# Kernel tuning notes

Hardware: AMD Instinct MI355X
Metric: run time of the kernel (lower is better)

The kernel has to match this reference:

```python
import jax, jax.numpy as jnp
import numpy as np

H = 1024          # hidden_size
NH = 16           # num_attention_heads
HD = H // NH      # head_size
EPS = 1e-5


def setup_inputs() -> dict:
    key = jax.random.key(0)
    ks = jax.random.split(key, 5)
    # xavier_uniform bound for Linear(in, out): sqrt(6/(in+out))
    b_qkv = float(np.sqrt(6.0 / (H + 3 * H)))
    b_out = float(np.sqrt(6.0 / (H + H)))
    return {
        "hidden_states": jax.random.normal(ks[0], (2, 2048, H), dtype=jnp.float32),
        "ln_gamma": jnp.ones((H,), jnp.float32),
        "ln_beta": jnp.zeros((H,), jnp.float32),
        "W_qkv": jax.random.uniform(ks[1], (3 * H, H), jnp.float32, -b_qkv, b_qkv),
        "b_qkv": jnp.zeros((3 * H,), jnp.float32),
        "W_out": jax.random.uniform(ks[2], (H, H), jnp.float32, -b_out, b_out),
        "b_out": jnp.zeros((H,), jnp.float32),
    }


def _attn_block(x, ln_gamma, ln_beta, W_qkv, b_qkv, W_out, b_out):
    B, S, _ = x.shape
    # Pre-LN
    mu = jnp.mean(x, axis=-1, keepdims=True)
    var = jnp.mean(jnp.square(x - mu), axis=-1, keepdims=True)
    xn = (x - mu) / jnp.sqrt(var + EPS) * ln_gamma + ln_beta
    # fused QKV projection: [B,S,3H]
    qkv = jnp.einsum("bsh,oh->bso", xn, W_qkv) + b_qkv
    qkv = qkv.reshape(B, S, 3, NH, HD).transpose(2, 0, 3, 1, 4)  # [3,B,NH,S,HD]
    q, k, v = qkv[0], qkv[1], qkv[2]
    scores = jnp.einsum("bhqd,bhkd->bhqk", q, k) / jnp.sqrt(jnp.asarray(HD, x.dtype))
    probs = jax.nn.softmax(scores, axis=-1)
    ctx = jnp.einsum("bhqk,bhkd->bhqd", probs, v)
    ctx = ctx.transpose(0, 2, 1, 3).reshape(B, S, H)
    out = jnp.einsum("bsh,oh->bso", ctx, W_out) + b_out  # dropout: eval mode = identity
    return x + out


def reference(hidden_states, ln_gamma, ln_beta, W_qkv, b_qkv, W_out, b_out):
    return _attn_block(hidden_states, ln_gamma, ln_beta, W_qkv, b_qkv, W_out, b_out)
```

## Files before the change

kernel.cpp:

```cpp
#include <hip/hip_runtime.h>
#include <stdint.h>

typedef unsigned short u16;
typedef __attribute__((ext_vector_type(8))) short bf16x8;
typedef __attribute__((ext_vector_type(4))) float f32x4;
typedef __attribute__((ext_vector_type(4))) unsigned int u32x4;
typedef __attribute__((ext_vector_type(2))) unsigned int u32x2;
typedef __attribute__((ext_vector_type(4))) unsigned short u16x4;

#define QSCALE 0.18033688011112042f

typedef __attribute__((address_space(1))) const void gvoid;
typedef __attribute__((address_space(3))) void svoid;

__device__ __forceinline__ void cp16(const u16* g, u16* l) {
    __builtin_amdgcn_global_load_lds((gvoid*)g, (svoid*)l, 16, 0, 0);
}

__device__ __forceinline__ u16 f2bf(float f) {
    uint32_t u = __float_as_uint(f);
    u += 0x7fff + ((u >> 16) & 1);
    return (u16)(u >> 16);
}

__device__ __forceinline__ uint32_t pack_bf2(float lo, float hi) {
    uint32_t a = __float_as_uint(lo) + 0x8000u;
    uint32_t b = __float_as_uint(hi) + 0x8000u;
    return __builtin_amdgcn_perm(b, a, 0x07060302);
}

__global__ __launch_bounds__(256) void k_pre(const float* __restrict__ X,
                                             const float* __restrict__ gam,
                                             const float* __restrict__ bet,
                                             u16* __restrict__ XN,
                                             const float* __restrict__ Wqkv, u16* __restrict__ Wq,
                                             const float* __restrict__ Wout, u16* __restrict__ Wo) {
    __shared__ float red[8];
    const int bid = blockIdx.x;
    if (bid < 4096) {
        int t = bid;
        const float4* xp = (const float4*)(X + (size_t)t * 1024);
        float4 x = xp[threadIdx.x];
        float s  = x.x + x.y + x.z + x.w;
        float s2 = x.x*x.x + x.y*x.y + x.z*x.z + x.w*x.w;
        #pragma unroll
        for (int off = 1; off < 64; off <<= 1) {
            s  += __shfl_xor(s,  off, 64);
            s2 += __shfl_xor(s2, off, 64);
        }
        int lane = threadIdx.x & 63, w = threadIdx.x >> 6;
        if (lane == 0) { red[w] = s; red[w + 4] = s2; }
        __syncthreads();
        s  = red[0] + red[1] + red[2] + red[3];
        s2 = red[4] + red[5] + red[6] + red[7];
        float mu  = s * (1.0f / 1024.0f);
        float var = s2 * (1.0f / 1024.0f) - mu * mu;
        float rin = rsqrtf(var + 1e-5f);
        float4 g = ((const float4*)gam)[threadIdx.x];
        float4 b = ((const float4*)bet)[threadIdx.x];
        u16x4 o;
        o.x = f2bf((x.x - mu) * rin * g.x + b.x);
        o.y = f2bf((x.y - mu) * rin * g.y + b.y);
        o.z = f2bf((x.z - mu) * rin * g.z + b.z);
        o.w = f2bf((x.w - mu) * rin * g.w + b.w);
        *(u16x4*)(XN + (size_t)t * 1024 + threadIdx.x * 4) = o;
    } else {
        int i = (bid - 4096) * 256 + threadIdx.x;
        const float* src; u16* dst;
        if (i < 786432) { src = Wqkv; dst = Wq; }
        else            { i -= 786432; src = Wout; dst = Wo; }
        float4 v = ((const float4*)src)[i];
        u16x4 o;
        o.x = f2bf(v.x); o.y = f2bf(v.y); o.z = f2bf(v.z); o.w = f2bf(v.w);
        ((u16x4*)dst)[i] = o;
    }
}

__device__ __forceinline__ void gemm_bt_tile(const u16* __restrict__ A, const u16* __restrict__ Bm,
                                             int m0, int n0, u16* As, u16* Bs, f32x4 acc[4][4]) {
    const int tid = threadIdx.x;
    const int lane = tid & 63;
    const int wv = tid >> 6;
    const int qi = lane & 15, g = lane >> 4, swz = qi & 7;
    const int wr = (wv >> 1) * 64, wc = (wv & 1) * 64;
    #pragma unroll
    for (int mi = 0; mi < 4; mi++)
        #pragma unroll
        for (int ni = 0; ni < 4; ni++) acc[mi][ni] = (f32x4){0.f, 0.f, 0.f, 0.f};

    const int row_in = tid >> 3;
    const int cs = (tid & 7) ^ (row_in & 7);
    for (int k0 = 0; k0 < 1024; k0 += 64) {
        __syncthreads();
        #pragma unroll
        for (int i = 0; i < 4; i++) {
            int row = i * 32 + row_in;
            cp16(A  + (size_t)(m0 + row) * 1024 + k0 + cs * 8, As + (i * 256 + wv * 64) * 8);
            cp16(Bm + (size_t)(n0 + row) * 1024 + k0 + cs * 8, Bs + (i * 256 + wv * 64) * 8);
        }
        __syncthreads();
        #pragma unroll
        for (int ks = 0; ks < 2; ks++) {
            bf16x8 af[4], bf[4];
            #pragma unroll
            for (int mi = 0; mi < 4; mi++)
                af[mi] = *(const bf16x8*)(As + (wr + mi * 16 + qi) * 64 + ((ks * 4 + g) ^ swz) * 8);
            #pragma unroll
            for (int ni = 0; ni < 4; ni++)
                bf[ni] = *(const bf16x8*)(Bs + (wc + ni * 16 + qi) * 64 + ((ks * 4 + g) ^ swz) * 8);
            #pragma unroll
            for (int mi = 0; mi < 4; mi++)
                #pragma unroll
                for (int ni = 0; ni < 4; ni++)
                    acc[mi][ni] = __builtin_amdgcn_mfma_f32_16x16x32_bf16(af[mi], bf[ni], acc[mi][ni], 0, 0, 0);
        }
    }
}

__global__ __launch_bounds__(256) void k_qkv(const u16* __restrict__ XN, const u16* __restrict__ Wq,
                                             const float* __restrict__ bqkv,
                                             u16* __restrict__ Q, u16* __restrict__ K,
                                             u16* __restrict__ Vt) {
    __shared__ __align__(16) u16 SMEM[17408];
    u16* As = SMEM;
    u16* Bs = SMEM + 8192;
    f32x4 acc[4][4];
    const int m0 = blockIdx.y * 128, n0 = blockIdx.x * 128;
    gemm_bt_tile(XN, Wq, m0, n0, As, Bs, acc);
    const int lane = threadIdx.x & 63, wid = threadIdx.x >> 6;
    const int g = lane >> 4, qi = lane & 15;
    const int wr = (wid >> 1) * 64, wc = (wid & 1) * 64;
    if (n0 < 2048) {
        const int which = n0 >> 10;
        u16* base = which ? K : Q;
        const float scale = which ? 1.0f : QSCALE;
        #pragma unroll
        for (int mi = 0; mi < 4; mi++)
            #pragma unroll
            for (int ni = 0; ni < 4; ni++)
                #pragma unroll
                for (int i = 0; i < 4; i++) {
                    int m = m0 + wr + mi * 16 + (g * 4 + i);
                    int n = n0 + wc + ni * 16 + qi;
                    float v = (acc[mi][ni][i] + bqkv[n]) * scale;
                    int b = m >> 11, s = m & 2047;
                    int hh = (n >> 6) & 15, d = n & 63;
                    base[((size_t)(b * 16 + hh) * 2048 + s) * 64 + d] = f2bf(v);
                }
    } else {
        __syncthreads();
        u16* Tw = SMEM + wid * 4352;
        #pragma unroll
        for (int mi = 0; mi < 4; mi++)
            #pragma unroll
            for (int ni = 0; ni < 4; ni++) {
                int n = n0 + wc + ni * 16 + qi;
                float bq = bqkv[n];
                u16x4 pk;
                pk.x = f2bf(acc[mi][ni][0] + bq);
                pk.y = f2bf(acc[mi][ni][1] + bq);
                pk.z = f2bf(acc[mi][ni][2] + bq);
                pk.w = f2bf(acc[mi][ni][3] + bq);
                *(u16x4*)(Tw + (ni * 16 + qi) * 68 + mi * 16 + g * 4) = pk;
            }
        const int head = (n0 + wc - 2048) >> 6;
        const int b = m0 >> 11;
        const int s0 = (m0 + wr) & 2047;
        u16* vrow = Vt + (size_t)(b * 16 + head) * 64 * 2048 + s0 + qi * 4;
        #pragma unroll
        for (int dd = 0; dd < 16; dd++) {
            int d = dd * 4 + g;
            u16x4 val = *(const u16x4*)(Tw + d * 68 + qi * 4);
            *(u16x4*)(vrow + (size_t)d * 2048) = val;
        }
    }
}

__global__ __launch_bounds__(512) void k_attn(const u16* __restrict__ Q, const u16* __restrict__ K,
                                              const u16* __restrict__ Vt, u16* __restrict__ CTX) {
    __shared__ __align__(16) u16 Ks[2][64 * 64];
    __shared__ __align__(16) u16 Vs[2][64 * 64];
    __shared__ __align__(16) u16 Ps[8][16 * 64];
    const int id = blockIdx.x;
    const int bh = (id & 7) * 4 + ((id >> 3) & 3);
    const int q0 = (id >> 5) * 128;
    const int lane = threadIdx.x & 63, w = threadIdx.x >> 6;
    const int g = lane >> 4, qi = lane & 15, swz = qi & 7;
    const u16* Qp = Q  + (size_t)bh * (2048 * 64);
    const u16* Kp = K  + (size_t)bh * (2048 * 64);
    const u16* Vp = Vt + (size_t)bh * (64 * 2048);
    u16* Pw = Ps[w];

    const int r0 = w * 8 + (lane >> 3);
    const int cs = (lane & 7) ^ (r0 & 7);
    const u16* kg0 = Kp + (size_t)r0 * 64 + cs * 8;
    const u16* vg0 = Vp + (size_t)r0 * 2048 + cs * 8;

    bf16x8 bq[2];
    {
        const u16* qb = Qp + (size_t)(q0 + w * 16 + qi) * 64 + g * 8;
        bq[0] = *(const bf16x8*)(qb);
        bq[1] = *(const bf16x8*)(qb + 32);
    }
    float lsumA = 0.f, lsumB = 0.f;
    f32x4 od[4];
    #pragma unroll
    for (int nt = 0; nt < 4; nt++) od[nt] = (f32x4){0.f, 0.f, 0.f, 0.f};

    cp16(kg0, Ks[0] + w * 512);
    cp16(vg0, Vs[0] + w * 512);

    #define ATTN_STEP(KT, CKS, CVS, PKS, PVS)                                                    \
    {                                                                                            \
        const int kt_ = (KT);                                                                    \
        __syncthreads();                                                                         \
        if (kt_ < 31) {                                                                          \
            cp16(kg0 + 4096, (PKS) + w * 512);                 \
            cp16(vg0 + 64,   (PVS) + w * 512);            \
        }                                                                                        \
        const u16* ksp = (CKS);                                                                  \
        const u16* vsp = (CVS);                                                                  \
        f32x4 sv[4];                                                                             \
        _Pragma("unroll")                                                                        \
        for (int nt = 0; nt < 4; nt++) sv[nt] = (f32x4){0.f, 0.f, 0.f, 0.f};                     \
        _Pragma("unroll")                                                                        \
        for (int ks = 0; ks < 2; ks++)                                                           \
            _Pragma("unroll")                                                                    \
            for (int nt = 0; nt < 4; nt++) {                                                     \
                bf16x8 ak = *(const bf16x8*)(ksp + (nt * 16 + qi) * 64 + ((ks * 4 + g) ^ swz) * 8); \
                sv[nt] = __builtin_amdgcn_mfma_f32_16x16x32_bf16(ak, bq[ks], sv[nt], 0, 0, 0);   \
            }                                                                                    \
        _Pragma("unroll")                                                                        \
        for (int nt = 0; nt < 2; nt++) {                                                         \
            float e0 = __builtin_amdgcn_exp2f(sv[nt][0]);                                        \
            float e1 = __builtin_amdgcn_exp2f(sv[nt][1]);                                        \
            float e2 = __builtin_amdgcn_exp2f(sv[nt][2]);                                        \
            float e3 = __builtin_amdgcn_exp2f(sv[nt][3]);                                        \
            lsumA += e0 + e1; lsumB += e2 + e3;                                                  \
            u32x2 pk = {pack_bf2(e0, e1), pack_bf2(e2, e3)};                                     \
            *(u32x2*)(Pw + qi * 64 + ((2 * nt + (g >> 1)) ^ swz) * 8 + (g & 1) * 4) = pk;        \
        }                                                                                        \
        {                                                                                        \
            bf16x8 bp = *(const bf16x8*)(Pw + qi * 64 + ((0 * 4 + g) ^ swz) * 8);                \
            _Pragma("unroll")                                                                    \
            for (int nt = 0; nt < 4; nt++) {                                                     \
                bf16x8 av = *(const bf16x8*)(vsp + (nt * 16 + qi) * 64 + ((0 * 4 + g) ^ swz) * 8); \
                od[nt] = __builtin_amdgcn_mfma_f32_16x16x32_bf16(av, bp, od[nt], 0, 0, 0);       \
            }                                                                                    \
        }                                                                                        \
        _Pragma("unroll")                                                                        \
        for (int nt = 2; nt < 4; nt++) {                                                         \
            float e0 = __builtin_amdgcn_exp2f(sv[nt][0]);                                        \
            float e1 = __builtin_amdgcn_exp2f(sv[nt][1]);                                        \
            float e2 = __builtin_amdgcn_exp2f(sv[nt][2]);                                        \
            float e3 = __builtin_amdgcn_exp2f(sv[nt][3]);                                        \
            lsumA += e0 + e1; lsumB += e2 + e3;                                                  \
            u32x2 pk = {pack_bf2(e0, e1), pack_bf2(e2, e3)};                                     \
            *(u32x2*)(Pw + qi * 64 + ((2 * nt + (g >> 1)) ^ swz) * 8 + (g & 1) * 4) = pk;        \
        }                                                                                        \
        {                                                                                        \
            bf16x8 bp = *(const bf16x8*)(Pw + qi * 64 + ((1 * 4 + g) ^ swz) * 8);                \
            _Pragma("unroll")                                                                    \
            for (int nt = 0; nt < 4; nt++) {                                                     \
                bf16x8 av = *(const bf16x8*)(vsp + (nt * 16 + qi) * 64 + ((1 * 4 + g) ^ swz) * 8); \
                od[nt] = __builtin_amdgcn_mfma_f32_16x16x32_bf16(av, bp, od[nt], 0, 0, 0);       \
            }                                                                                    \
        }                                                                                        \
        kg0 += 64 * 64; vg0 += 64;                                                               \
    }

    for (int kt = 0; kt < 32; kt += 2) {
        ATTN_STEP(kt,     Ks[0], Vs[0], Ks[1], Vs[1]);
        ATTN_STEP(kt + 1, Ks[1], Vs[1], Ks[0], Vs[0]);
    }
    #undef ATTN_STEP

    float lsum = lsumA + lsumB;
    lsum += __shfl_xor(lsum, 16, 64);
    lsum += __shfl_xor(lsum, 32, 64);
    float inv = 1.0f / lsum;
    const int b = bh >> 4, hh = bh & 15;
    size_t m = (size_t)b * 2048 + q0 + w * 16 + qi;
    u16* cp = CTX + m * 1024 + hh * 64 + g * 4;
    #pragma unroll
    for (int nt = 0; nt < 4; nt++) {
        u16x4 o;
        o.x = f2bf(od[nt][0] * inv); o.y = f2bf(od[nt][1] * inv);
        o.z = f2bf(od[nt][2] * inv); o.w = f2bf(od[nt][3] * inv);
        *(u16x4*)(cp + nt * 16) = o;
    }
}

__global__ __launch_bounds__(256) void k_out(const u16* __restrict__ CTX, const u16* __restrict__ Wo,
                                             const float* __restrict__ bout, const float* __restrict__ X,
                                             float* __restrict__ OUT) {
    __shared__ __align__(16) u16 As[128 * 64], Bs[128 * 64];
    f32x4 acc[4][4];
    const int m0 = blockIdx.y * 128, n0 = blockIdx.x * 128;
    gemm_bt_tile(CTX, Wo, m0, n0, As, Bs, acc);
    const int lane = threadIdx.x & 63, wid = threadIdx.x >> 6;
    const int wr = (wid >> 1) * 64, wc = (wid & 1) * 64;
    #pragma unroll
    for (int mi = 0; mi < 4; mi++)
        #pragma unroll
        for (int ni = 0; ni < 4; ni++)
            #pragma unroll
            for (int i = 0; i < 4; i++) {
                size_t m = m0 + wr + mi * 16 + ((lane >> 4) * 4 + i);
                int n = n0 + wc + ni * 16 + (lane & 15);
                OUT[m * 1024 + n] = acc[mi][ni][i] + bout[n] + X[m * 1024 + n];
            }
}

extern "C" void kernel_launch(void* const* d_in, const int* in_sizes, int n_in,
                              void* d_out, int out_size, void* d_ws, size_t ws_size,
                              hipStream_t stream) {
    const float* X    = (const float*)d_in[0];
    const float* gam  = (const float*)d_in[1];
    const float* bet  = (const float*)d_in[2];
    const float* Wqkv = (const float*)d_in[3];
    const float* bqkv = (const float*)d_in[4];
    const float* Wout = (const float*)d_in[5];
    const float* bout = (const float*)d_in[6];
    float* OUT = (float*)d_out;

    u16* XN  = (u16*)d_ws;
    u16* Q   = XN  + (size_t)4 * 1024 * 1024;
    u16* K   = Q   + (size_t)4 * 1024 * 1024;
    u16* Vt  = K   + (size_t)4 * 1024 * 1024;
    u16* CTX = Vt  + (size_t)4 * 1024 * 1024;
    u16* Wq  = CTX + (size_t)4 * 1024 * 1024;
    u16* Wo  = Wq  + (size_t)3 * 1024 * 1024;

    k_pre<<<8192, 256, 0, stream>>>(X, gam, bet, XN, Wqkv, Wq, Wout, Wo);
    k_qkv<<<dim3(24, 32), 256, 0, stream>>>(XN, Wq, bqkv, Q, K, Vt);
    k_attn<<<512, 512, 0, stream>>>(Q, K, Vt, CTX);
    k_out<<<dim3(8, 32), 256, 0, stream>>>(CTX, Wo, bout, X, OUT);
}
```

Baseline: 200.6 us.

## Rewrite QKV GEMM as 256x256 tile with double-buffered phased pipeline

The QKV projection kernel moves from 128x128 tiles with 256 threads to 256x256 tiles with 512 threads and a swizzled 1D grid of 192 blocks. Its main loop becomes a hand-scheduled double-buffered pipeline: async global-to-LDS copies for the next k-steps are issued between MFMA phases, with explicit vmcnt/lgkmcnt waits, barriers and setprio around the MFMA bursts. The goal is more data reuse per tile and hiding load latency behind matrix math. In exchange it uses 128KB of LDS and 32 accumulators per thread, which raises register pressure and may limit occupancy. The V-transpose epilogue is split into two halves to fit the larger tile.

```diff
diff --git a/kernel.cpp b/kernel.cpp
--- a/kernel.cpp
+++ b/kernel.cpp
@@ -117,25 +117,116 @@
     }
 }
 
-__global__ __launch_bounds__(256) void k_qkv(const u16* __restrict__ XN, const u16* __restrict__ Wq,
-                                             const float* __restrict__ bqkv,
-                                             u16* __restrict__ Q, u16* __restrict__ K,
-                                             u16* __restrict__ Vt) {
-    __shared__ __align__(16) u16 SMEM[17408];
-    u16* As = SMEM;
-    u16* Bs = SMEM + 8192;
-    f32x4 acc[4][4];
-    const int m0 = blockIdx.y * 128, n0 = blockIdx.x * 128;
-    gemm_bt_tile(XN, Wq, m0, n0, As, Bs, acc);
-    const int lane = threadIdx.x & 63, wid = threadIdx.x >> 6;
-    const int g = lane >> 4, qi = lane & 15;
-    const int wr = (wid >> 1) * 64, wc = (wid & 1) * 64;
+
+#define CFENCE asm volatile("" ::: "memory")
+#define BARX() do { CFENCE; __builtin_amdgcn_s_barrier(); CFENCE; } while (0)
+#define LGKM0() asm volatile("s_waitcnt lgkmcnt(0)" ::: "memory")
+
+__global__ __launch_bounds__(512, 2) void k_qkv(const u16* __restrict__ XN, const u16* __restrict__ Wq,
+                                                const float* __restrict__ bqkv,
+                                                u16* __restrict__ Q, u16* __restrict__ K,
+                                                u16* __restrict__ Vt) {
+    __shared__ __align__(16) u16 SMEM[65536];
+    const int tid = threadIdx.x;
+    const int lane = tid & 63, w = tid >> 6;
+    const int qi = lane & 15, g = lane >> 4, swz = qi & 7;
+    const int wr = (w >> 2) * 128, wc = (w & 3) * 64;
+
+    const int id = blockIdx.x;
+    const int sw = (id & 7) * 24 + (id >> 3);
+    const int n0 = (sw % 12) * 256;
+    const int m0 = (sw / 12) * 256;
+
+    const int laneRow = lane >> 3, laneCg = lane & 7;
+    const int cs = laneCg ^ laneRow;
+    const int aw = (w & 3) * 8 + (w >> 2) * 128;
+    const u16* gA = XN + (size_t)(m0 + aw + laneRow) * 1024 + cs * 8;
+    const u16* gB = Wq + (size_t)(n0 + w * 8 + laneRow) * 1024 + cs * 8;
+
+#define SM_A(s) (SMEM + (s) * 32768)
+#define SM_B(s) (SMEM + (s) * 32768 + 16384)
+#define STAGE_A(tau, q, s) cp16(gA + (size_t)(q) * 32 * 1024 + (tau) * 64, SM_A(s) + ((q) * 32 + aw) * 64)
+#define STAGE_B(tau, part, s)                                                                       \
+    do { cp16(gB + (size_t)(part) * 128 * 1024 + (tau) * 64, SM_B(s) + ((part) * 128 + w * 8) * 64); \
+         cp16(gB + (size_t)((part) * 128 + 64) * 1024 + (tau) * 64,                                  \
+              SM_B(s) + ((part) * 128 + 64 + w * 8) * 64); } while (0)
+
+    f32x4 acc[8][4];
+    #pragma unroll
+    for (int mi = 0; mi < 8; mi++)
+        #pragma unroll
+        for (int ni = 0; ni < 4; ni++) acc[mi][ni] = (f32x4){0.f, 0.f, 0.f, 0.f};
+    bf16x8 bf[4][2];
+
+    STAGE_B(0, 0, 0); STAGE_B(0, 1, 0);
+    STAGE_A(0, 0, 0); STAGE_A(0, 1, 0); STAGE_A(0, 2, 0); STAGE_A(0, 3, 0);
+    STAGE_B(1, 0, 1); STAGE_B(1, 1, 1);
+    STAGE_A(1, 0, 1); STAGE_A(1, 1, 1);
+    asm volatile("s_waitcnt vmcnt(6)" ::: "memory");
+    BARX();
+
+#define PHASE_A(q)                                                                                   \
+    bf16x8 af[2][2];                                                                                 \
+    _Pragma("unroll") for (int m2 = 0; m2 < 2; m2++)                                                 \
+    _Pragma("unroll") for (int ks = 0; ks < 2; ks++)                                                 \
+        af[m2][ks] = *(const bf16x8*)(as_ + (wr + ((q) * 2 + m2) * 16 + qi) * 64 + (((ks * 4 + g) ^ swz)) * 8);
+
+#define DO_MFMA(q)                                                                                   \
+    __builtin_amdgcn_s_setprio(1);                                                                   \
+    _Pragma("unroll") for (int m2 = 0; m2 < 2; m2++)                                                 \
+    _Pragma("unroll") for (int ni = 0; ni < 4; ni++) {                                               \
+        acc[(q) * 2 + m2][ni] = __builtin_amdgcn_mfma_f32_16x16x32_bf16(af[m2][0], bf[ni][0], acc[(q) * 2 + m2][ni], 0, 0, 0); \
+        acc[(q) * 2 + m2][ni] = __builtin_amdgcn_mfma_f32_16x16x32_bf16(af[m2][1], bf[ni][1], acc[(q) * 2 + m2][ni], 0, 0, 0); \
+    }                                                                                                \
+    __builtin_amdgcn_s_setprio(0);
+
+    for (int t = 0; t < 16; t++) {
+        const int s = t & 1;
+        const u16* as_ = SM_A(s);
+        const u16* bs_ = SM_B(s);
+        {
+            PHASE_A(0)
+            #pragma unroll
+            for (int ni = 0; ni < 4; ni++)
+                #pragma unroll
+                for (int ks = 0; ks < 2; ks++)
+                    bf[ni][ks] = *(const bf16x8*)(bs_ + (wc + ni * 16 + qi) * 64 + ((ks * 4 + g) ^ swz) * 8);
+            if (t < 15) { STAGE_A(t + 1, 2, s ^ 1); STAGE_A(t + 1, 3, s ^ 1); }
+            BARX(); LGKM0();
+            DO_MFMA(0)
+            BARX();
+        }
+        {
+            PHASE_A(1)
+            if (t < 14) STAGE_B(t + 2, 0, s);
+            BARX(); LGKM0();
+            DO_MFMA(1)
+            BARX();
+        }
+        {
+            PHASE_A(2)
+            if (t < 14) STAGE_B(t + 2, 1, s);
+            BARX(); LGKM0();
+            DO_MFMA(2)
+            BARX();
+        }
+        {
+            PHASE_A(3)
+            if (t < 14) { STAGE_A(t + 2, 0, s); STAGE_A(t + 2, 1, s); }
+            BARX(); LGKM0();
+            DO_MFMA(3)
+            if (t < 14) { asm volatile("s_waitcnt vmcnt(6)" ::: "memory"); }
+            else        { asm volatile("s_waitcnt vmcnt(0)" ::: "memory"); }
+            BARX();
+        }
+    }
+
     if (n0 < 2048) {
         const int which = n0 >> 10;
         u16* base = which ? K : Q;
         const float scale = which ? 1.0f : QSCALE;
         #pragma unroll
-        for (int mi = 0; mi < 4; mi++)
+        for (int mi = 0; mi < 8; mi++)
             #pragma unroll
             for (int ni = 0; ni < 4; ni++)
                 #pragma unroll
@@ -143,37 +234,46 @@
                     int m = m0 + wr + mi * 16 + (g * 4 + i);
                     int n = n0 + wc + ni * 16 + qi;
                     float v = (acc[mi][ni][i] + bqkv[n]) * scale;
-                    int b = m >> 11, s = m & 2047;
+                    int b = m >> 11, ss = m & 2047;
                     int hh = (n >> 6) & 15, d = n & 63;
-                    base[((size_t)(b * 16 + hh) * 2048 + s) * 64 + d] = f2bf(v);
+                    base[((size_t)(b * 16 + hh) * 2048 + ss) * 64 + d] = f2bf(v);
                 }
     } else {
-        __syncthreads();
-        u16* Tw = SMEM + wid * 4352;
-        #pragma unroll
-        for (int mi = 0; mi < 4; mi++)
-            #pragma unroll
-            for (int ni = 0; ni < 4; ni++) {
-                int n = n0 + wc + ni * 16 + qi;
-                float bq = bqkv[n];
-                u16x4 pk;
-                pk.x = f2bf(acc[mi][ni][0] + bq);
-                pk.y = f2bf(acc[mi][ni][1] + bq);
-                pk.z = f2bf(acc[mi][ni][2] + bq);
-                pk.w = f2bf(acc[mi][ni][3] + bq);
-                *(u16x4*)(Tw + (ni * 16 + qi) * 68 + mi * 16 + g * 4) = pk;
-            }
+        u16* Tw = SMEM + w * 4352;
         const int head = (n0 + wc - 2048) >> 6;
         const int b = m0 >> 11;
-        const int s0 = (m0 + wr) & 2047;
-        u16* vrow = Vt + (size_t)(b * 16 + head) * 64 * 2048 + s0 + qi * 4;
-        #pragma unroll
-        for (int dd = 0; dd < 16; dd++) {
-            int d = dd * 4 + g;
-            u16x4 val = *(const u16x4*)(Tw + d * 68 + qi * 4);
-            *(u16x4*)(vrow + (size_t)d * 2048) = val;
-        }
-    }
+        #pragma unroll
+        for (int h = 0; h < 2; h++) {
+            #pragma unroll
+            for (int mi2 = 0; mi2 < 4; mi2++)
+                #pragma unroll
+                for (int ni = 0; ni < 4; ni++) {
+                    int mi = h * 4 + mi2;
+                    int n = n0 + wc + ni * 16 + qi;
+                    float bq = bqkv[n];
+                    u16x4 pk;
+                    pk.x = f2bf(acc[mi][ni][0] + bq);
+                    pk.y = f2bf(acc[mi][ni][1] + bq);
+                    pk.z = f2bf(acc[mi][ni][2] + bq);
+                    pk.w = f2bf(acc[mi][ni][3] + bq);
+                    *(u16x4*)(Tw + (ni * 16 + qi) * 68 + mi2 * 16 + g * 4) = pk;
+                }
+            int s0 = (m0 + wr + h * 64) & 2047;
+            u16* vrow = Vt + (size_t)(b * 16 + head) * 64 * 2048 + s0 + qi * 4;
+            #pragma unroll
+            for (int dd = 0; dd < 16; dd++) {
+                int d = dd * 4 + g;
+                u16x4 val = *(const u16x4*)(Tw + d * 68 + qi * 4);
+                *(u16x4*)(vrow + (size_t)d * 2048) = val;
+            }
+        }
+    }
+#undef SM_A
+#undef SM_B
+#undef STAGE_A
+#undef STAGE_B
+#undef PHASE_A
+#undef DO_MFMA
 }
 
 __global__ __launch_bounds__(512) void k_attn(const u16* __restrict__ Q, const u16* __restrict__ K,
@@ -333,7 +433,7 @@
     u16* Wo  = Wq  + (size_t)3 * 1024 * 1024;
 
     k_pre<<<8192, 256, 0, stream>>>(X, gam, bet, XN, Wqkv, Wq, Wout, Wo);
-    k_qkv<<<dim3(24, 32), 256, 0, stream>>>(XN, Wq, bqkv, Q, K, Vt);
+    k_qkv<<<192, 512, 0, stream>>>(XN, Wq, bqkv, Q, K, Vt);
     k_attn<<<512, 512, 0, stream>>>(Q, K, Vt, CTX);
     k_out<<<dim3(8, 32), 256, 0, stream>>>(CTX, Wo, bout, X, OUT);
 }
```

Measured after the change: 190.6 us. -5.0%, faster.
